# Kernel optimization log

Measured on AMD Instinct MI355X. Metric: run time of the kernel, lower is better.

Reference implementation:

```python
import jax, jax.numpy as jnp
import numpy as np

B, I, H = 4096, 1024, 1024


def setup_inputs() -> dict:
    key = jax.random.key(0)
    ks = jax.random.split(key, 7)
    s = 0.1  # matches uniform(-0.1, 0.1) init scale loosely
    return {
        "input": jax.random.normal(ks[0], (B, I), jnp.float32),
        "h_t": jax.random.normal(ks[1], (B, H), jnp.float32),
        "c_t": jax.random.normal(ks[2], (B, H), jnp.float32),
        "w_i": jax.random.uniform(ks[3], (I, 4 * H), jnp.float32, -s, s),
        "w_h": jax.random.uniform(ks[4], (H, 4 * H), jnp.float32, -s, s),
        "b_i": jax.random.uniform(ks[5], (4 * H,), jnp.float32, -s, s),
        "b_h": jax.random.uniform(ks[6], (4 * H,), jnp.float32, -s, s),
    }


def reference(input, h_t, c_t, w_i, w_h, b_i, b_h):
    # ifgo: [B, 4H] = x @ w_i + h @ w_h + b_i + b_h
    ifgo = input @ w_i + h_t @ w_h + (b_i + b_h)
    i, f, g, o = jnp.split(ifgo, 4, axis=1)
    i = jax.nn.sigmoid(i)
    f = jax.nn.sigmoid(f)
    g = jnp.tanh(g)
    o = jax.nn.sigmoid(o)
    c_new = f * c_t + i * g
    h_new = o * jnp.tanh(c_new)
    return (h_new, c_new)
```

## Files before the change

kernel.cpp:

```cpp
#include <hip/hip_runtime.h>
#include <stdint.h>

typedef __attribute__((ext_vector_type(8))) short short8;
typedef __attribute__((ext_vector_type(4))) float floatx4;

__device__ inline unsigned short f2bf(float x) {
  union { float f; unsigned int u; } v; v.f = x;
  unsigned int r = v.u + 0x7FFFu + ((v.u >> 16) & 1u);
  return (unsigned short)(r >> 16);
}

__global__ void pack_all(const float* __restrict__ x, const float* __restrict__ h,
                         const float* __restrict__ wi, const float* __restrict__ wh,
                         unsigned short* __restrict__ A,
                         unsigned short* __restrict__ Wt) {
  int bid = blockIdx.x;
  int t = threadIdx.x;
  if (bid < 4096) {
    int idx = bid * 256 + t;
    int row = idx >> 8;
    int kc  = (idx & 255) << 3;
    const float* src = (kc < 1024) ? (x + (size_t)row * 1024 + kc)
                                   : (h + (size_t)row * 1024 + (kc - 1024));
    float4 a = ((const float4*)src)[0];
    float4 b = ((const float4*)src)[1];
    uint4 o;
    o.x = f2bf(a.x) | ((unsigned)f2bf(a.y) << 16);
    o.y = f2bf(a.z) | ((unsigned)f2bf(a.w) << 16);
    o.z = f2bf(b.x) | ((unsigned)f2bf(b.y) << 16);
    o.w = f2bf(b.z) | ((unsigned)f2bf(b.w) << 16);
    *(uint4*)(A + (size_t)row * 2048 + kc) = o;
  } else {
    __shared__ float tile[64][65];
    int b2 = bid - 4096;
    int kt = b2 & 31;
    int nt = b2 >> 5;
    int k0 = kt << 6, n0 = nt << 6;
    const float* src = (k0 < 1024) ? (wi + (size_t)k0 * 4096)
                                   : (wh + (size_t)(k0 - 1024) * 4096);
    int c4 = (t & 15) << 2, rr = t >> 4;
#pragma unroll
    for (int p = 0; p < 4; ++p) {
      int kk = rr + p * 16;
      float4 v = *(const float4*)(src + (size_t)kk * 4096 + n0 + c4);
      tile[kk][c4 + 0] = v.x; tile[kk][c4 + 1] = v.y;
      tile[kk][c4 + 2] = v.z; tile[kk][c4 + 3] = v.w;
    }
    __syncthreads();
    int k8 = (t & 7) << 3, nn = t >> 3;
#pragma unroll
    for (int p = 0; p < 2; ++p) {
      int n = n0 + nn + p * 32;
      int hh = n & 1023, g = n >> 10;
      int R = ((hh >> 5) << 7) + (((hh >> 4) & 1) << 6) + (g << 4) + (hh & 15);
      int nl = nn + p * 32;
      uint4 o;
      o.x = f2bf(tile[k8 + 0][nl]) | ((unsigned)f2bf(tile[k8 + 1][nl]) << 16);
      o.y = f2bf(tile[k8 + 2][nl]) | ((unsigned)f2bf(tile[k8 + 3][nl]) << 16);
      o.z = f2bf(tile[k8 + 4][nl]) | ((unsigned)f2bf(tile[k8 + 5][nl]) << 16);
      o.w = f2bf(tile[k8 + 6][nl]) | ((unsigned)f2bf(tile[k8 + 7][nl]) << 16);
      *(uint4*)(Wt + (size_t)R * 2048 + k0 + k8) = o;
    }
  }
}

__device__ inline void gl_lds16(const void* g, void* l) {
  __builtin_amdgcn_global_load_lds(
      (const __attribute__((address_space(1))) void*)g,
      (__attribute__((address_space(3))) void*)l, 16, 0, 0);
}

__device__ inline float sigm(float x)  { return 1.0f / (1.0f + __expf(-x)); }
__device__ inline float tanhx(float x) { return 2.0f / (1.0f + __expf(-2.0f * x)) - 1.0f; }

__global__ void gemm_lstm(const unsigned short* __restrict__ A,
                          const unsigned short* __restrict__ Bt,
                          const float* __restrict__ ct,
                          const float* __restrict__ bi,
                          const float* __restrict__ bh,
                          float* __restrict__ out) {
  constexpr int K = 2048;
  __shared__ char AsB[128 * 64];
  __shared__ char BsB[128 * 64];
  const int tid  = threadIdx.x;
  const int lane = tid & 63;
  const int wave = tid >> 6;
  const int wm = wave >> 1, wn = wave & 1;
  const int m0 = blockIdx.y << 7;
  const int n0 = blockIdx.x << 7;
  const int h0 = blockIdx.x << 5;

  const int er = (lane >> 4) << 2;
  const int ec = lane & 15;
  const int h  = h0 + (wn << 4) + ec;
  float bias[4];
#pragma unroll
  for (int j = 0; j < 4; ++j) bias[j] = bi[j * 1024 + h] + bh[j * 1024 + h];
  float cpre[4][4];
#pragma unroll
  for (int i = 0; i < 4; ++i)
#pragma unroll
    for (int rg = 0; rg < 4; ++rg) {
      int row = m0 + (wm << 6) + i * 16 + er + rg;
      cpre[i][rg] = ct[(size_t)row * 1024 + h];
    }

  const int r  = tid >> 2;
  const int cb = (tid & 3) << 4;
  const char* aS0 = (const char*)A + (size_t)(m0 + r) * K * 2 + cb;
  const char* aS1 = aS0 + (size_t)64 * K * 2;
  const char* bS0 = (const char*)Bt + (size_t)(n0 + r) * K * 2 + cb;
  const char* bS1 = bS0 + (size_t)64 * K * 2;
  char* aD0 = AsB + tid * 16;
  char* aD1 = AsB + 4096 + tid * 16;
  char* bD0 = BsB + tid * 16;
  char* bD1 = BsB + 4096 + tid * 16;

  floatx4 acc[4][4] = {};
  const int rA = (wm << 6) + (lane & 15);
  const int rB = (wn << 6) + (lane & 15);
  const int kb = (lane >> 4) << 4;

  for (int ks = 0; ks < K; ks += 32) {
    gl_lds16(aS0, aD0); gl_lds16(aS1, aD1);
    gl_lds16(bS0, bD0); gl_lds16(bS1, bD1);
    aS0 += 64; aS1 += 64; bS0 += 64; bS1 += 64;
    __syncthreads();
    short8 af[4], bfr[4];
#pragma unroll
    for (int f = 0; f < 4; ++f) {
      af[f]  = *(const short8*)(AsB + (rA + f * 16) * 64 + kb);
      bfr[f] = *(const short8*)(BsB + (rB + f * 16) * 64 + kb);
    }
#pragma unroll
    for (int i = 0; i < 4; ++i)
#pragma unroll
      for (int j = 0; j < 4; ++j)
        acc[i][j] = __builtin_amdgcn_mfma_f32_16x16x32_bf16(af[i], bfr[j], acc[i][j], 0, 0, 0);
    __syncthreads();
  }

#pragma unroll
  for (int i = 0; i < 4; ++i) {
#pragma unroll
    for (int rg = 0; rg < 4; ++rg) {
      int row = m0 + (wm << 6) + i * 16 + er + rg;
      size_t o = (size_t)row * 1024 + h;
      float iv = sigm(acc[i][0][rg] + bias[0]);
      float fv = sigm(acc[i][1][rg] + bias[1]);
      float gv = tanhx(acc[i][2][rg] + bias[2]);
      float ov = sigm(acc[i][3][rg] + bias[3]);
      float cn = fv * cpre[i][rg] + iv * gv;
      out[o] = ov * tanhx(cn);
      out[4194304 + o] = cn;
    }
  }
}

extern "C" void kernel_launch(void* const* d_in, const int* in_sizes, int n_in,
                              void* d_out, int out_size, void* d_ws, size_t ws_size,
                              hipStream_t stream) {
  const float* x  = (const float*)d_in[0];
  const float* ht = (const float*)d_in[1];
  const float* ct = (const float*)d_in[2];
  const float* wi = (const float*)d_in[3];
  const float* wh = (const float*)d_in[4];
  const float* bi = (const float*)d_in[5];
  const float* bh = (const float*)d_in[6];
  float* out = (float*)d_out;

  char* ws = (char*)d_ws;
  unsigned short* Abf = (unsigned short*)ws;
  unsigned short* Wbf = (unsigned short*)(ws + (16u << 20));

  pack_all<<<6144, 256, 0, stream>>>(x, ht, wi, wh, Abf, Wbf);
  gemm_lstm<<<dim3(32, 32), 256, 0, stream>>>(Abf, Wbf, ct, bi, bh, out);
}
```

Baseline: 225.2 us.

## Double K-step per iteration with XOR-swizzled LDS and late c_t load

Each main-loop iteration now covers 64 K elements instead of 32, halving the number of barrier pairs. The global-to-LDS copies use an XOR swizzle on 16-byte columns, and fragment reads apply the matching swizzle to avoid LDS bank conflicts on the 128-byte rows. The c_t values are loaded after the GEMM loop rather than before it, which frees registers during the main loop, and the kernel gets launch_bounds(256). Cost is twice the LDS per block, which may lower occupancy, and still no double buffering.

```diff
diff --git a/kernel.cpp b/kernel.cpp
--- a/kernel.cpp
+++ b/kernel.cpp
@@ -73,15 +73,16 @@
 __device__ inline float sigm(float x)  { return 1.0f / (1.0f + __expf(-x)); }
 __device__ inline float tanhx(float x) { return 2.0f / (1.0f + __expf(-2.0f * x)) - 1.0f; }
 
-__global__ void gemm_lstm(const unsigned short* __restrict__ A,
-                          const unsigned short* __restrict__ Bt,
-                          const float* __restrict__ ct,
-                          const float* __restrict__ bi,
-                          const float* __restrict__ bh,
-                          float* __restrict__ out) {
+__global__ void __launch_bounds__(256) gemm_lstm(
+    const unsigned short* __restrict__ A,
+    const unsigned short* __restrict__ Bt,
+    const float* __restrict__ ct,
+    const float* __restrict__ bi,
+    const float* __restrict__ bh,
+    float* __restrict__ out) {
   constexpr int K = 2048;
-  __shared__ char AsB[128 * 64];
-  __shared__ char BsB[128 * 64];
+  __shared__ char AsB[128 * 128];
+  __shared__ char BsB[128 * 128];
   const int tid  = threadIdx.x;
   const int lane = tid & 63;
   const int wave = tid >> 6;
@@ -96,50 +97,70 @@
   float bias[4];
 #pragma unroll
   for (int j = 0; j < 4; ++j) bias[j] = bi[j * 1024 + h] + bh[j * 1024 + h];
-  float cpre[4][4];
+
+  const int sr = tid >> 3;
+  const int cs = ((tid & 7) ^ (sr & 7)) << 4;
+  const char* aS[4];
+  const char* bS[4];
+#pragma unroll
+  for (int p = 0; p < 4; ++p) {
+    aS[p] = (const char*)A  + (size_t)(m0 + p * 32 + sr) * K * 2 + cs;
+    bS[p] = (const char*)Bt + (size_t)(n0 + p * 32 + sr) * K * 2 + cs;
+  }
+  char* aD = AsB + tid * 16;
+  char* bD = BsB + tid * 16;
+
+  floatx4 acc[4][4] = {};
+  const int rA = (wm << 6) + (lane & 15);
+  const int rB = (wn << 6) + (lane & 15);
+  const int keyc = lane & 7;
+  const int kq   = lane >> 4;
+  const int c0 = ((kq ^ keyc) << 4);
+  const int c1 = (((4 + kq) ^ keyc) << 4);
+
+  for (int ks = 0; ks < K; ks += 64) {
+#pragma unroll
+    for (int p = 0; p < 4; ++p) { gl_lds16(aS[p], aD + p * 4096); aS[p] += 128; }
+#pragma unroll
+    for (int p = 0; p < 4; ++p) { gl_lds16(bS[p], bD + p * 4096); bS[p] += 128; }
+    __syncthreads();
+    {
+      short8 af[4], bfr[4];
+#pragma unroll
+      for (int f = 0; f < 4; ++f) {
+        af[f]  = *(const short8*)(AsB + (rA + f * 16) * 128 + c0);
+        bfr[f] = *(const short8*)(BsB + (rB + f * 16) * 128 + c0);
+      }
+#pragma unroll
+      for (int i = 0; i < 4; ++i)
+#pragma unroll
+        for (int j = 0; j < 4; ++j)
+          acc[i][j] = __builtin_amdgcn_mfma_f32_16x16x32_bf16(af[i], bfr[j], acc[i][j], 0, 0, 0);
+    }
+    {
+      short8 af[4], bfr[4];
+#pragma unroll
+      for (int f = 0; f < 4; ++f) {
+        af[f]  = *(const short8*)(AsB + (rA + f * 16) * 128 + c1);
+        bfr[f] = *(const short8*)(BsB + (rB + f * 16) * 128 + c1);
+      }
+#pragma unroll
+      for (int i = 0; i < 4; ++i)
+#pragma unroll
+        for (int j = 0; j < 4; ++j)
+          acc[i][j] = __builtin_amdgcn_mfma_f32_16x16x32_bf16(af[i], bfr[j], acc[i][j], 0, 0, 0);
+    }
+    __syncthreads();
+  }
+
+  float cv[4][4];
 #pragma unroll
   for (int i = 0; i < 4; ++i)
 #pragma unroll
     for (int rg = 0; rg < 4; ++rg) {
       int row = m0 + (wm << 6) + i * 16 + er + rg;
-      cpre[i][rg] = ct[(size_t)row * 1024 + h];
+      cv[i][rg] = ct[(size_t)row * 1024 + h];
     }
-
-  const int r  = tid >> 2;
-  const int cb = (tid & 3) << 4;
-  const char* aS0 = (const char*)A + (size_t)(m0 + r) * K * 2 + cb;
-  const char* aS1 = aS0 + (size_t)64 * K * 2;
-  const char* bS0 = (const char*)Bt + (size_t)(n0 + r) * K * 2 + cb;
-  const char* bS1 = bS0 + (size_t)64 * K * 2;
-  char* aD0 = AsB + tid * 16;
-  char* aD1 = AsB + 4096 + tid * 16;
-  char* bD0 = BsB + tid * 16;
-  char* bD1 = BsB + 4096 + tid * 16;
-
-  floatx4 acc[4][4] = {};
-  const int rA = (wm << 6) + (lane & 15);
-  const int rB = (wn << 6) + (lane & 15);
-  const int kb = (lane >> 4) << 4;
-
-  for (int ks = 0; ks < K; ks += 32) {
-    gl_lds16(aS0, aD0); gl_lds16(aS1, aD1);
-    gl_lds16(bS0, bD0); gl_lds16(bS1, bD1);
-    aS0 += 64; aS1 += 64; bS0 += 64; bS1 += 64;
-    __syncthreads();
-    short8 af[4], bfr[4];
-#pragma unroll
-    for (int f = 0; f < 4; ++f) {
-      af[f]  = *(const short8*)(AsB + (rA + f * 16) * 64 + kb);
-      bfr[f] = *(const short8*)(BsB + (rB + f * 16) * 64 + kb);
-    }
-#pragma unroll
-    for (int i = 0; i < 4; ++i)
-#pragma unroll
-      for (int j = 0; j < 4; ++j)
-        acc[i][j] = __builtin_amdgcn_mfma_f32_16x16x32_bf16(af[i], bfr[j], acc[i][j], 0, 0, 0);
-    __syncthreads();
-  }
-
 #pragma unroll
   for (int i = 0; i < 4; ++i) {
 #pragma unroll
@@ -150,7 +171,7 @@
       float fv = sigm(acc[i][1][rg] + bias[1]);
       float gv = tanhx(acc[i][2][rg] + bias[2]);
       float ov = sigm(acc[i][3][rg] + bias[3]);
-      float cn = fv * cpre[i][rg] + iv * gv;
+      float cn = fv * cv[i][rg] + iv * gv;
       out[o] = ov * tanhx(cn);
       out[4194304 + o] = cn;
     }
```

Result: faster. 204.9 us (-9.0%).
